# Optimization experiments

Measured on AMD Instinct MI355X. Metric: run time of the kernel, lower is better.

The kernel has to match this reference:

```python
import jax, jax.numpy as jnp
import numpy as np

N = 100000   # nodes
E = 800000   # edges
D = 64       # feature dim (input=hidden=output)
EPS = 1e-5   # BatchNorm eps


def setup_inputs() -> dict:
    key = jax.random.key(0)
    ks = jax.random.split(key, 24)
    s = 1.0 / np.sqrt(D)
    inp = {
        "x": jax.random.normal(ks[0], (N, D), jnp.float32),
        "edge_index": jax.random.randint(ks[1], (2, E), 0, N, jnp.int64),
        # GCNConv weights (x @ W + b after normalized aggregation)
        "W1": jax.random.normal(ks[2], (D, D), jnp.float32) * s,
        "b1": jax.random.normal(ks[3], (D,), jnp.float32) * 0.01,
        "W2": jax.random.normal(ks[4], (D, D), jnp.float32) * s,
        "b2": jax.random.normal(ks[5], (D,), jnp.float32) * 0.01,
        "W3": jax.random.normal(ks[6], (D, D), jnp.float32) * s,
        "b3": jax.random.normal(ks[7], (D,), jnp.float32) * 0.01,
        # BatchNorm1d (inference: running stats)
        "bn1_g": jax.random.uniform(ks[8], (D,), jnp.float32, 0.5, 1.5),
        "bn1_b": jax.random.normal(ks[9], (D,), jnp.float32) * 0.1,
        "bn1_m": jax.random.normal(ks[10], (D,), jnp.float32) * 0.1,
        "bn1_v": jax.random.uniform(ks[11], (D,), jnp.float32, 0.5, 1.5),
        "bn2_g": jax.random.uniform(ks[12], (D,), jnp.float32, 0.5, 1.5),
        "bn2_b": jax.random.normal(ks[13], (D,), jnp.float32) * 0.1,
        "bn2_m": jax.random.normal(ks[14], (D,), jnp.float32) * 0.1,
        "bn2_v": jax.random.uniform(ks[15], (D,), jnp.float32, 0.5, 1.5),
        # predictor MLP: Linear -> tanh -> (dropout=id) -> Linear
        "pW1": jax.random.normal(ks[16], (D, D), jnp.float32) * s,
        "pb1": jax.random.normal(ks[17], (D,), jnp.float32) * 0.01,
        "pW2": jax.random.normal(ks[18], (D, D), jnp.float32) * s,
        "pb2": jax.random.normal(ks[19], (D,), jnp.float32) * 0.01,
    }
    return inp


def _gcn_norm(edge_index):
    # add self loops, compute sym-normalized edge coefficients (PyG GCNConv)
    loop = jnp.arange(N, dtype=edge_index.dtype)
    src = jnp.concatenate([edge_index[0], loop])
    dst = jnp.concatenate([edge_index[1], loop])
    deg = jax.ops.segment_sum(jnp.ones(src.shape[0], jnp.float32), dst, num_segments=N)
    dis = jax.lax.rsqrt(deg)  # deg >= 1 due to self loops
    norm = dis[src] * dis[dst]
    return src, dst, norm


def _gcn_layer(x, src, dst, norm, W, b):
    h = x @ W                              # [N, D] small GEMM
    msg = h[src] * norm[:, None]           # [E+N, D] gather (memory bound)
    return jax.ops.segment_sum(msg, dst, num_segments=N) + b  # scatter-add


def _bn(x, g, b, m, v):
    return (x - m) * (g * jax.lax.rsqrt(v + EPS)) + b


def reference(x, edge_index, W1, b1, W2, b2, W3, b3,
              bn1_g, bn1_b, bn1_m, bn1_v, bn2_g, bn2_b, bn2_m, bn2_v,
              pW1, pb1, pW2, pb2):
    src, dst, norm = _gcn_norm(edge_index)
    h = _gcn_layer(x, src, dst, norm, W1, b1)
    h = jax.nn.relu(_bn(h, bn1_g, bn1_b, bn1_m, bn1_v))   # dropout = id (eval)
    h = _gcn_layer(h, src, dst, norm, W2, b2)
    h = jax.nn.relu(_bn(h, bn2_g, bn2_b, bn2_m, bn2_v))
    h = _gcn_layer(h, src, dst, norm, W3, b3)
    out = jnp.tanh(h @ pW1 + pb1) @ pW2 + pb2              # predictor MLP
    return out
```

## Files before the change

kernel.cpp:

```cpp
#include <hip/hip_runtime.h>
#include <hip/hip_fp16.h>

#define N_NODES 100000
#define N_EDGES 800000
#define DIM 64
#define BN_EPS 1e-5f
#define LDX 68
#define EDGE_CAP 1600000

__global__ __launch_bounds__(256) void k_cvt_count(const float* __restrict__ x,
                                                   __half* __restrict__ xh,
                                                   const int* __restrict__ dst,
                                                   int* __restrict__ deg) {
    int idx = blockIdx.x * blockDim.x + threadIdx.x;
    if (idx < 1600000) {
        float4 v = ((const float4*)x)[idx];
        unsigned int u0 = __half_as_ushort(__float2half(v.x));
        unsigned int u1 = __half_as_ushort(__float2half(v.y));
        unsigned int u2 = __half_as_ushort(__float2half(v.z));
        unsigned int u3 = __half_as_ushort(__float2half(v.w));
        ((uint2*)xh)[idx] = make_uint2(u0 | (u1 << 16), u2 | (u3 << 16));
    }
    if (idx < N_EDGES) atomicAdd(&deg[dst[idx]], 1);
}

__global__ __launch_bounds__(256) void k_scan_fuse(const int* __restrict__ deg,
                                                   int* __restrict__ row_off,
                                                   int* __restrict__ cursor,
                                                   float* __restrict__ dinv,
                                                   int* __restrict__ gcount,
                                                   const float* __restrict__ W3,
                                                   const float* __restrict__ b3,
                                                   const float* __restrict__ pW1,
                                                   const float* __restrict__ pb1,
                                                   float* __restrict__ W3p,
                                                   float* __restrict__ b3p) {
    int tid = threadIdx.x;
    if (blockIdx.x == 98) {
        int c = tid & 63;
        int kbase = (tid >> 6) * 16;
        for (int k = kbase; k < kbase + 16; ++k) {
            float acc = 0.f;
#pragma unroll 8
            for (int j = 0; j < 64; ++j)
                acc = fmaf(W3[k * 64 + j], pW1[j * 64 + c], acc);
            W3p[k * 64 + c] = acc;
        }
        if (tid < 64) {
            float acc = pb1[c];
#pragma unroll 8
            for (int j = 0; j < 64; ++j)
                acc = fmaf(b3[j], pW1[j * 64 + c], acc);
            b3p[c] = acc;
        }
        return;
    }
    __shared__ int sdata[256];
    __shared__ int sbase;
    int base = blockIdx.x * 1024 + tid * 4;
    int4 d = make_int4(0, 0, 0, 0);
    int4 v = make_int4(0, 0, 0, 0);
    if (base < N_NODES) {
        d = *(const int4*)(deg + base);
        v.x = (d.x + 7) & ~7;
        v.y = (d.y + 7) & ~7;
        v.z = (d.z + 7) & ~7;
        v.w = (d.w + 7) & ~7;
    }
    int tsum = v.x + v.y + v.z + v.w;
    sdata[tid] = tsum;
    __syncthreads();
    for (int off = 1; off < 256; off <<= 1) {
        int t = (tid >= off) ? sdata[tid - off] : 0;
        __syncthreads();
        sdata[tid] += t;
        __syncthreads();
    }
    if (tid == 255) sbase = atomicAdd(gcount, sdata[255]);
    __syncthreads();
    if (base >= N_NODES) return;
    int excl = sdata[tid] - tsum + sbase;
    int4 o;
    o.x = excl;
    o.y = o.x + v.x;
    o.z = o.y + v.y;
    o.w = o.z + v.z;
    *(int4*)(row_off + base) = o;
    *(int4*)(cursor + base) = o;
    float4 di;
    di.x = rsqrtf((float)(d.x + 1));
    di.y = rsqrtf((float)(d.y + 1));
    di.z = rsqrtf((float)(d.z + 1));
    di.w = rsqrtf((float)(d.w + 1));
    *(float4*)(dinv + base) = di;
}

__global__ __launch_bounds__(256) void k_build(const int* __restrict__ ei,
                                               const float* __restrict__ dinv,
                                               int* __restrict__ cursor,
                                               int2* __restrict__ edges) {
    int e = blockIdx.x * blockDim.x + threadIdx.x;
    if (e >= N_EDGES) return;
    int s = ei[e];
    int d = ei[N_EDGES + e];
    int pos = atomicAdd(&cursor[d], 1);
    edges[pos] = make_int2(s, __float_as_int(dinv[s] * dinv[d]));
}

__global__ __launch_bounds__(256) void k_aggregate(const __half* __restrict__ xin,
                                                   const int* __restrict__ row_off,
                                                   const int* __restrict__ deg,
                                                   const int2* __restrict__ edges,
                                                   const float* __restrict__ dinv,
                                                   __half* __restrict__ out) {
    int lane = threadIdx.x & 63;
    int node = blockIdx.x * 4 + (threadIdx.x >> 6);
    float di = dinv[node];
    float acc = __half2float(xin[(size_t)node * DIM + lane]) * (di * di);
    int beg = __builtin_amdgcn_readfirstlane(row_off[node]);
    int lenp = (__builtin_amdgcn_readfirstlane(deg[node]) + 7) & ~7;
    int end = beg + lenp;
    for (int k = beg; k < end; k += 8) {
        int2 e0 = edges[k + 0];
        int2 e1 = edges[k + 1];
        int2 e2 = edges[k + 2];
        int2 e3 = edges[k + 3];
        int2 e4 = edges[k + 4];
        int2 e5 = edges[k + 5];
        int2 e6 = edges[k + 6];
        int2 e7 = edges[k + 7];
        float v0 = __half2float(xin[(size_t)e0.x * DIM + lane]);
        float v1 = __half2float(xin[(size_t)e1.x * DIM + lane]);
        float v2 = __half2float(xin[(size_t)e2.x * DIM + lane]);
        float v3 = __half2float(xin[(size_t)e3.x * DIM + lane]);
        float v4 = __half2float(xin[(size_t)e4.x * DIM + lane]);
        float v5 = __half2float(xin[(size_t)e5.x * DIM + lane]);
        float v6 = __half2float(xin[(size_t)e6.x * DIM + lane]);
        float v7 = __half2float(xin[(size_t)e7.x * DIM + lane]);
        acc = fmaf(__int_as_float(e0.y), v0, acc);
        acc = fmaf(__int_as_float(e1.y), v1, acc);
        acc = fmaf(__int_as_float(e2.y), v2, acc);
        acc = fmaf(__int_as_float(e3.y), v3, acc);
        acc = fmaf(__int_as_float(e4.y), v4, acc);
        acc = fmaf(__int_as_float(e5.y), v5, acc);
        acc = fmaf(__int_as_float(e6.y), v6, acc);
        acc = fmaf(__int_as_float(e7.y), v7, acc);
    }
    out[(size_t)node * DIM + lane] = __float2half(acc);
}

#define GEMM_STEP(SX, SW)                                                      \
    {                                                                          \
        float4 a0 = *(const float4*)&SX[(r0 + 0) * LDX + k4 * 4];              \
        float4 a1 = *(const float4*)&SX[(r0 + 1) * LDX + k4 * 4];              \
        float4 a2 = *(const float4*)&SX[(r0 + 2) * LDX + k4 * 4];              \
        float4 a3 = *(const float4*)&SX[(r0 + 3) * LDX + k4 * 4];              \
        float4 b0 = *(const float4*)&SW[(k4 * 4 + 0) * 64 + c0];               \
        float4 b1 = *(const float4*)&SW[(k4 * 4 + 1) * 64 + c0];               \
        float4 b2 = *(const float4*)&SW[(k4 * 4 + 2) * 64 + c0];               \
        float4 b3 = *(const float4*)&SW[(k4 * 4 + 3) * 64 + c0];               \
        const float* ap[4] = {&a0.x, &a1.x, &a2.x, &a3.x};                     \
        _Pragma("unroll") for (int i = 0; i < 4; ++i) {                        \
            float x0 = ap[i][0], x1 = ap[i][1], x2 = ap[i][2], x3 = ap[i][3];  \
            acc[i][0] = fmaf(x0, b0.x, acc[i][0]);                             \
            acc[i][1] = fmaf(x0, b0.y, acc[i][1]);                             \
            acc[i][2] = fmaf(x0, b0.z, acc[i][2]);                             \
            acc[i][3] = fmaf(x0, b0.w, acc[i][3]);                             \
            acc[i][0] = fmaf(x1, b1.x, acc[i][0]);                             \
            acc[i][1] = fmaf(x1, b1.y, acc[i][1]);                             \
            acc[i][2] = fmaf(x1, b1.z, acc[i][2]);                             \
            acc[i][3] = fmaf(x1, b1.w, acc[i][3]);                             \
            acc[i][0] = fmaf(x2, b2.x, acc[i][0]);                             \
            acc[i][1] = fmaf(x2, b2.y, acc[i][1]);                             \
            acc[i][2] = fmaf(x2, b2.z, acc[i][2]);                             \
            acc[i][3] = fmaf(x2, b2.w, acc[i][3]);                             \
            acc[i][0] = fmaf(x3, b3.x, acc[i][0]);                             \
            acc[i][1] = fmaf(x3, b3.y, acc[i][1]);                             \
            acc[i][2] = fmaf(x3, b3.z, acc[i][2]);                             \
            acc[i][3] = fmaf(x3, b3.w, acc[i][3]);                             \
        }                                                                      \
    }

#define STAGE_H2F(SRCPTR, SXPTR)                                               \
    {                                                                          \
        int r = tid >> 2;                                                      \
        int q = tid & 3;                                                       \
        int row = row0 + r;                                                    \
        float4* dst = (float4*)(SXPTR + r * LDX);                              \
        if (row < N_NODES) {                                                   \
            const uint2* src = (const uint2*)(SRCPTR + (size_t)row * DIM);     \
            _Pragma("unroll") for (int m = 0; m < 4; ++m) {                    \
                uint2 u = src[q + m * 4];                                      \
                float4 f;                                                      \
                f.x = __half2float(__ushort_as_half((unsigned short)(u.x & 0xffff)));       \
                f.y = __half2float(__ushort_as_half((unsigned short)(u.x >> 16)));          \
                f.z = __half2float(__ushort_as_half((unsigned short)(u.y & 0xffff)));       \
                f.w = __half2float(__ushort_as_half((unsigned short)(u.y >> 16)));          \
                dst[q + m * 4] = f;                                            \
            }                                                                  \
        } else {                                                               \
            float4 z = make_float4(0.f, 0.f, 0.f, 0.f);                        \
            _Pragma("unroll") for (int m = 0; m < 4; ++m) dst[q + m * 4] = z;  \
        }                                                                      \
    }

__global__ __launch_bounds__(256) void k_gemm_bn_h(const __half* __restrict__ xin,
                                                   const float* __restrict__ W,
                                                   const float* __restrict__ bias,
                                                   const float* __restrict__ bng,
                                                   const float* __restrict__ bnb,
                                                   const float* __restrict__ bnm,
                                                   const float* __restrict__ bnv,
                                                   __half* __restrict__ out) {
    __shared__ float sW[4096];
    __shared__ float sX[64 * LDX];
    int tid = threadIdx.x;
    int row0 = blockIdx.x * 64;

    for (int i = tid; i < 1024; i += 256)
        ((float4*)sW)[i] = ((const float4*)W)[i];
    STAGE_H2F(xin, sX)
    __syncthreads();

    int cq = tid & 15, rq = tid >> 4;
    int c0 = cq * 4, r0 = rq * 4;
    float acc[4][4];
#pragma unroll
    for (int i = 0; i < 4; ++i)
#pragma unroll
        for (int j = 0; j < 4; ++j) acc[i][j] = 0.f;

#pragma unroll 4
    for (int k4 = 0; k4 < 16; ++k4) GEMM_STEP(sX, sW)

    float4 bv = *(const float4*)&bias[c0];
    float4 g = *(const float4*)&bng[c0];
    float4 bb = *(const float4*)&bnb[c0];
    float4 m = *(const float4*)&bnm[c0];
    float4 vv = *(const float4*)&bnv[c0];
    float A0 = g.x * rsqrtf(vv.x + BN_EPS);
    float A1 = g.y * rsqrtf(vv.y + BN_EPS);
    float A2 = g.z * rsqrtf(vv.z + BN_EPS);
    float A3 = g.w * rsqrtf(vv.w + BN_EPS);
    float B0 = (bv.x - m.x) * A0 + bb.x;
    float B1 = (bv.y - m.y) * A1 + bb.y;
    float B2 = (bv.z - m.z) * A2 + bb.z;
    float B3 = (bv.w - m.w) * A3 + bb.w;
#pragma unroll
    for (int i = 0; i < 4; ++i) {
        int row = row0 + r0 + i;
        if (row >= N_NODES) break;
        unsigned int u0 = __half_as_ushort(__float2half(fmaxf(0.f, fmaf(acc[i][0], A0, B0))));
        unsigned int u1 = __half_as_ushort(__float2half(fmaxf(0.f, fmaf(acc[i][1], A1, B1))));
        unsigned int u2 = __half_as_ushort(__float2half(fmaxf(0.f, fmaf(acc[i][2], A2, B2))));
        unsigned int u3 = __half_as_ushort(__float2half(fmaxf(0.f, fmaf(acc[i][3], A3, B3))));
        *(uint2*)(out + (size_t)row * DIM + c0) = make_uint2(u0 | (u1 << 16), u2 | (u3 << 16));
    }
}

__global__ __launch_bounds__(256) void k_tail(const __half* __restrict__ xin,
                                              const float* __restrict__ W3p,
                                              const float* __restrict__ b3p,
                                              const float* __restrict__ pW2,
                                              const float* __restrict__ pb2,
                                              float* __restrict__ out) {
    __shared__ float sW1[4096];
    __shared__ float sW2[4096];
    __shared__ float sX[64 * LDX];
    int tid = threadIdx.x;
    int row0 = blockIdx.x * 64;

    for (int i = tid; i < 1024; i += 256) {
        ((float4*)sW1)[i] = ((const float4*)W3p)[i];
        ((float4*)sW2)[i] = ((const float4*)pW2)[i];
    }
    STAGE_H2F(xin, sX)
    __syncthreads();

    int cq = tid & 15, rq = tid >> 4;
    int c0 = cq * 4, r0 = rq * 4;
    float acc[4][4];

#pragma unroll
    for (int i = 0; i < 4; ++i)
#pragma unroll
        for (int j = 0; j < 4; ++j) acc[i][j] = 0.f;
#pragma unroll 4
    for (int k4 = 0; k4 < 16; ++k4) GEMM_STEP(sX, sW1)
    __syncthreads();

    {
        float4 bv = *(const float4*)&b3p[c0];
#pragma unroll
        for (int i = 0; i < 4; ++i) {
            float4 h;
            h.x = tanhf(acc[i][0] + bv.x);
            h.y = tanhf(acc[i][1] + bv.y);
            h.z = tanhf(acc[i][2] + bv.z);
            h.w = tanhf(acc[i][3] + bv.w);
            *(float4*)&sX[(r0 + i) * LDX + c0] = h;
        }
    }
    __syncthreads();

#pragma unroll
    for (int i = 0; i < 4; ++i)
#pragma unroll
        for (int j = 0; j < 4; ++j) acc[i][j] = 0.f;
#pragma unroll 4
    for (int k4 = 0; k4 < 16; ++k4) GEMM_STEP(sX, sW2)

    float4 bv = *(const float4*)&pb2[c0];
#pragma unroll
    for (int i = 0; i < 4; ++i) {
        int row = row0 + r0 + i;
        if (row >= N_NODES) break;
        float4 o;
        o.x = acc[i][0] + bv.x;
        o.y = acc[i][1] + bv.y;
        o.z = acc[i][2] + bv.z;
        o.w = acc[i][3] + bv.w;
        *(float4*)(out + (size_t)row * DIM + c0) = o;
    }
}

extern "C" void kernel_launch(void* const* d_in, const int* in_sizes, int n_in,
                              void* d_out, int out_size, void* d_ws, size_t ws_size,
                              hipStream_t stream) {
    const float* x     = (const float*)d_in[0];
    const int*   ei    = (const int*)d_in[1];
    const float* W1    = (const float*)d_in[2];
    const float* b1    = (const float*)d_in[3];
    const float* W2    = (const float*)d_in[4];
    const float* b2    = (const float*)d_in[5];
    const float* W3    = (const float*)d_in[6];
    const float* b3    = (const float*)d_in[7];
    const float* bn1_g = (const float*)d_in[8];
    const float* bn1_b = (const float*)d_in[9];
    const float* bn1_m = (const float*)d_in[10];
    const float* bn1_v = (const float*)d_in[11];
    const float* bn2_g = (const float*)d_in[12];
    const float* bn2_b = (const float*)d_in[13];
    const float* bn2_m = (const float*)d_in[14];
    const float* bn2_v = (const float*)d_in[15];
    const float* pW1   = (const float*)d_in[16];
    const float* pb1   = (const float*)d_in[17];
    const float* pW2   = (const float*)d_in[18];
    const float* pb2   = (const float*)d_in[19];
    float* out = (float*)d_out;

    char* ws = (char*)d_ws;
    int*   deg      = (int*)ws;                      ws += 100352 * 4;
    int*   gcount   = (int*)ws;                      ws += 4 * 4;
    int*   row_off  = (int*)ws;                      ws += 100352 * 4;
    int*   cursor   = (int*)ws;                      ws += 100352 * 4;
    int2*  edges    = (int2*)ws;                     ws += (size_t)EDGE_CAP * 8;
    float* dinv     = (float*)ws;                    ws += 100352 * 4;
    float* W3p      = (float*)ws;                    ws += 4096 * 4;
    float* b3p      = (float*)ws;                    ws += 64 * 4;
    __half* xh      = (__half*)ws;                   ws += (size_t)N_NODES * DIM * 2;
    __half* hbuf    = (__half*)ws;                   ws += (size_t)N_NODES * DIM * 2;
    __half* abuf    = (__half*)ws;                   ws += (size_t)N_NODES * DIM * 2;

    const int blk = 256;
    int gE    = (N_EDGES + blk - 1) / blk;
    int gCvt  = 6250;
    int gAgg  = N_NODES / 4;
    int gTile = (N_NODES + 63) / 64;

    size_t zbytes = (size_t)(100352 * 3 + 4) * 4 + (size_t)EDGE_CAP * 8;
    hipMemsetAsync(deg, 0, zbytes, stream);
    k_cvt_count<<<gCvt, blk, 0, stream>>>(x, xh, ei + N_EDGES, deg);
    k_scan_fuse<<<99, blk, 0, stream>>>(deg, row_off, cursor, dinv, gcount,
                                        W3, b3, pW1, pb1, W3p, b3p);
    k_build<<<gE, blk, 0, stream>>>(ei, dinv, cursor, edges);

    k_aggregate<<<gAgg, blk, 0, stream>>>(xh, row_off, deg, edges, dinv, abuf);
    k_gemm_bn_h<<<gTile, blk, 0, stream>>>(abuf, W1, b1, bn1_g, bn1_b, bn1_m, bn1_v, hbuf);

    k_aggregate<<<gAgg, blk, 0, stream>>>(hbuf, row_off, deg, edges, dinv, abuf);
    k_gemm_bn_h<<<gTile, blk, 0, stream>>>(abuf, W2, b2, bn2_g, bn2_b, bn2_m, bn2_v, hbuf);

    k_aggregate<<<gAgg, blk, 0, stream>>>(hbuf, row_off, deg, edges, dinv, abuf);
    k_tail<<<gTile, blk, 0, stream>>>(abuf, W3p, b3p, pW2, pb2, out);
}
```

Measured before the change: 372.9 us.

## Factor symmetric GCN normalization into node scaling and shrink edge list to indices

Splits the symmetric edge weight dinv[s]*dinv[d] into per-node factors. Source features are pre-scaled by dinv, in the build kernel for the input and in the GEMM epilogue for hidden layers, and each aggregate result is multiplied by dinv[dst] once. The edge list then stores only a source index (offset by one so padded zero entries point at a zeroed sentinel row), halving edge bytes read in each of three aggregations and turning per-edge FMAs into adds. It adds an extra scaling pass over the input features, pads the feature buffers by a row, and uses separate ping-pong hidden buffers.

```diff
diff --git a/kernel.cpp b/kernel.cpp
--- a/kernel.cpp
+++ b/kernel.cpp
@@ -7,6 +7,7 @@
 #define BN_EPS 1e-5f
 #define LDX 68
 #define EDGE_CAP 1600000
+
 
 __global__ __launch_bounds__(256) void k_cvt_count(const float* __restrict__ x,
                                                    __half* __restrict__ xh,
@@ -19,8 +20,10 @@
         unsigned int u1 = __half_as_ushort(__float2half(v.y));
         unsigned int u2 = __half_as_ushort(__float2half(v.z));
         unsigned int u3 = __half_as_ushort(__float2half(v.w));
-        ((uint2*)xh)[idx] = make_uint2(u0 | (u1 << 16), u2 | (u3 << 16));
-    }
+        ((uint2*)(xh + DIM))[idx] = make_uint2(u0 | (u1 << 16), u2 | (u3 << 16));
+    }
+    if (blockIdx.x == 0 && threadIdx.x < 16)
+        ((uint2*)xh)[threadIdx.x] = make_uint2(0u, 0u);
     if (idx < N_EDGES) atomicAdd(&deg[dst[idx]], 1);
 }
 
@@ -95,58 +98,69 @@
     *(float4*)(dinv + base) = di;
 }
 
-__global__ __launch_bounds__(256) void k_build(const int* __restrict__ ei,
-                                               const float* __restrict__ dinv,
-                                               int* __restrict__ cursor,
-                                               int2* __restrict__ edges) {
-    int e = blockIdx.x * blockDim.x + threadIdx.x;
-    if (e >= N_EDGES) return;
-    int s = ei[e];
-    int d = ei[N_EDGES + e];
-    int pos = atomicAdd(&cursor[d], 1);
-    edges[pos] = make_int2(s, __float_as_int(dinv[s] * dinv[d]));
+__global__ __launch_bounds__(256) void k_build_scale(const int* __restrict__ ei,
+                                                     int* __restrict__ cursor,
+                                                     int* __restrict__ edges,
+                                                     const float* __restrict__ dinv,
+                                                     __half* __restrict__ xh) {
+    int b = blockIdx.x;
+    int tid = threadIdx.x;
+    if (b < 3125) {
+        int e = b * 256 + tid;
+        if (e >= N_EDGES) return;
+        int s = ei[e];
+        int d = ei[N_EDGES + e];
+        int pos = atomicAdd(&cursor[d], 1);
+        edges[pos] = s + 1;
+    } else {
+        int idx = (b - 3125) * 256 + tid;
+        int row = idx >> 4;
+        float dv = dinv[row];
+        uint2 u = ((uint2*)(xh + DIM))[idx];
+        float f0 = __half2float(__ushort_as_half((unsigned short)(u.x & 0xffff))) * dv;
+        float f1 = __half2float(__ushort_as_half((unsigned short)(u.x >> 16))) * dv;
+        float f2 = __half2float(__ushort_as_half((unsigned short)(u.y & 0xffff))) * dv;
+        float f3 = __half2float(__ushort_as_half((unsigned short)(u.y >> 16))) * dv;
+        unsigned int u0 = __half_as_ushort(__float2half(f0));
+        unsigned int u1 = __half_as_ushort(__float2half(f1));
+        unsigned int u2 = __half_as_ushort(__float2half(f2));
+        unsigned int u3 = __half_as_ushort(__float2half(f3));
+        ((uint2*)(xh + DIM))[idx] = make_uint2(u0 | (u1 << 16), u2 | (u3 << 16));
+    }
 }
 
 __global__ __launch_bounds__(256) void k_aggregate(const __half* __restrict__ xin,
                                                    const int* __restrict__ row_off,
                                                    const int* __restrict__ deg,
-                                                   const int2* __restrict__ edges,
+                                                   const int* __restrict__ edges,
                                                    const float* __restrict__ dinv,
                                                    __half* __restrict__ out) {
     int lane = threadIdx.x & 63;
     int node = blockIdx.x * 4 + (threadIdx.x >> 6);
-    float di = dinv[node];
-    float acc = __half2float(xin[(size_t)node * DIM + lane]) * (di * di);
+    float acc = __half2float(xin[(size_t)(node + 1) * DIM + lane]);
     int beg = __builtin_amdgcn_readfirstlane(row_off[node]);
     int lenp = (__builtin_amdgcn_readfirstlane(deg[node]) + 7) & ~7;
     int end = beg + lenp;
     for (int k = beg; k < end; k += 8) {
-        int2 e0 = edges[k + 0];
-        int2 e1 = edges[k + 1];
-        int2 e2 = edges[k + 2];
-        int2 e3 = edges[k + 3];
-        int2 e4 = edges[k + 4];
-        int2 e5 = edges[k + 5];
-        int2 e6 = edges[k + 6];
-        int2 e7 = edges[k + 7];
-        float v0 = __half2float(xin[(size_t)e0.x * DIM + lane]);
-        float v1 = __half2float(xin[(size_t)e1.x * DIM + lane]);
-        float v2 = __half2float(xin[(size_t)e2.x * DIM + lane]);
-        float v3 = __half2float(xin[(size_t)e3.x * DIM + lane]);
-        float v4 = __half2float(xin[(size_t)e4.x * DIM + lane]);
-        float v5 = __half2float(xin[(size_t)e5.x * DIM + lane]);
-        float v6 = __half2float(xin[(size_t)e6.x * DIM + lane]);
-        float v7 = __half2float(xin[(size_t)e7.x * DIM + lane]);
-        acc = fmaf(__int_as_float(e0.y), v0, acc);
-        acc = fmaf(__int_as_float(e1.y), v1, acc);
-        acc = fmaf(__int_as_float(e2.y), v2, acc);
-        acc = fmaf(__int_as_float(e3.y), v3, acc);
-        acc = fmaf(__int_as_float(e4.y), v4, acc);
-        acc = fmaf(__int_as_float(e5.y), v5, acc);
-        acc = fmaf(__int_as_float(e6.y), v6, acc);
-        acc = fmaf(__int_as_float(e7.y), v7, acc);
-    }
-    out[(size_t)node * DIM + lane] = __float2half(acc);
+        int e0 = edges[k + 0];
+        int e1 = edges[k + 1];
+        int e2 = edges[k + 2];
+        int e3 = edges[k + 3];
+        int e4 = edges[k + 4];
+        int e5 = edges[k + 5];
+        int e6 = edges[k + 6];
+        int e7 = edges[k + 7];
+        float v0 = __half2float(xin[(size_t)e0 * DIM + lane]);
+        float v1 = __half2float(xin[(size_t)e1 * DIM + lane]);
+        float v2 = __half2float(xin[(size_t)e2 * DIM + lane]);
+        float v3 = __half2float(xin[(size_t)e3 * DIM + lane]);
+        float v4 = __half2float(xin[(size_t)e4 * DIM + lane]);
+        float v5 = __half2float(xin[(size_t)e5 * DIM + lane]);
+        float v6 = __half2float(xin[(size_t)e6 * DIM + lane]);
+        float v7 = __half2float(xin[(size_t)e7 * DIM + lane]);
+        acc += ((v0 + v1) + (v2 + v3)) + ((v4 + v5) + (v6 + v7));
+    }
+    out[(size_t)node * DIM + lane] = __float2half(dinv[node] * acc);
 }
 
 #define GEMM_STEP(SX, SW)                                                      \
@@ -211,11 +225,15 @@
                                                    const float* __restrict__ bnb,
                                                    const float* __restrict__ bnm,
                                                    const float* __restrict__ bnv,
+                                                   const float* __restrict__ dinv,
                                                    __half* __restrict__ out) {
     __shared__ float sW[4096];
     __shared__ float sX[64 * LDX];
     int tid = threadIdx.x;
     int row0 = blockIdx.x * 64;
+
+    if (blockIdx.x == 0 && tid < 16)
+        ((uint2*)out)[tid] = make_uint2(0u, 0u);
 
     for (int i = tid; i < 1024; i += 256)
         ((float4*)sW)[i] = ((const float4*)W)[i];
@@ -250,11 +268,12 @@
     for (int i = 0; i < 4; ++i) {
         int row = row0 + r0 + i;
         if (row >= N_NODES) break;
-        unsigned int u0 = __half_as_ushort(__float2half(fmaxf(0.f, fmaf(acc[i][0], A0, B0))));
-        unsigned int u1 = __half_as_ushort(__float2half(fmaxf(0.f, fmaf(acc[i][1], A1, B1))));
-        unsigned int u2 = __half_as_ushort(__float2half(fmaxf(0.f, fmaf(acc[i][2], A2, B2))));
-        unsigned int u3 = __half_as_ushort(__float2half(fmaxf(0.f, fmaf(acc[i][3], A3, B3))));
-        *(uint2*)(out + (size_t)row * DIM + c0) = make_uint2(u0 | (u1 << 16), u2 | (u3 << 16));
+        float dv = dinv[row];
+        unsigned int u0 = __half_as_ushort(__float2half(fmaxf(0.f, fmaf(acc[i][0], A0, B0)) * dv));
+        unsigned int u1 = __half_as_ushort(__float2half(fmaxf(0.f, fmaf(acc[i][1], A1, B1)) * dv));
+        unsigned int u2 = __half_as_ushort(__float2half(fmaxf(0.f, fmaf(acc[i][2], A2, B2)) * dv));
+        unsigned int u3 = __half_as_ushort(__float2half(fmaxf(0.f, fmaf(acc[i][3], A3, B3)) * dv));
+        *(uint2*)(out + (size_t)(row + 1) * DIM + c0) = make_uint2(u0 | (u1 << 16), u2 | (u3 << 16));
     }
 }
 
@@ -350,37 +369,38 @@
     float* out = (float*)d_out;
 
     char* ws = (char*)d_ws;
-    int*   deg      = (int*)ws;                      ws += 100352 * 4;
-    int*   gcount   = (int*)ws;                      ws += 4 * 4;
-    int*   row_off  = (int*)ws;                      ws += 100352 * 4;
-    int*   cursor   = (int*)ws;                      ws += 100352 * 4;
-    int2*  edges    = (int2*)ws;                     ws += (size_t)EDGE_CAP * 8;
-    float* dinv     = (float*)ws;                    ws += 100352 * 4;
-    float* W3p      = (float*)ws;                    ws += 4096 * 4;
-    float* b3p      = (float*)ws;                    ws += 64 * 4;
-    __half* xh      = (__half*)ws;                   ws += (size_t)N_NODES * DIM * 2;
-    __half* hbuf    = (__half*)ws;                   ws += (size_t)N_NODES * DIM * 2;
+    int*    deg     = (int*)ws;                      ws += 100352 * 4;
+    int*    gcount  = (int*)ws;                      ws += 4 * 4;
+    int*    row_off = (int*)ws;                      ws += 100352 * 4;
+    int*    cursor  = (int*)ws;                      ws += 100352 * 4;
+    int*    edges   = (int*)ws;                      ws += (size_t)EDGE_CAP * 4;
+    float*  dinv    = (float*)ws;                    ws += 100352 * 4;
+    float*  W3p     = (float*)ws;                    ws += 4096 * 4;
+    float*  b3p     = (float*)ws;                    ws += 64 * 4;
+    __half* xh      = (__half*)ws;                   ws += (size_t)(N_NODES + 4) * DIM * 2;
+    __half* hbufA   = (__half*)ws;                   ws += (size_t)(N_NODES + 4) * DIM * 2;
+    __half* hbufB   = (__half*)ws;                   ws += (size_t)(N_NODES + 4) * DIM * 2;
     __half* abuf    = (__half*)ws;                   ws += (size_t)N_NODES * DIM * 2;
 
     const int blk = 256;
-    int gE    = (N_EDGES + blk - 1) / blk;
     int gCvt  = 6250;
+    int gBS   = 3125 + 6250;
     int gAgg  = N_NODES / 4;
     int gTile = (N_NODES + 63) / 64;
 
-    size_t zbytes = (size_t)(100352 * 3 + 4) * 4 + (size_t)EDGE_CAP * 8;
+    size_t zbytes = (size_t)(100352 * 3 + 4) * 4 + (size_t)EDGE_CAP * 4;
     hipMemsetAsync(deg, 0, zbytes, stream);
     k_cvt_count<<<gCvt, blk, 0, stream>>>(x, xh, ei + N_EDGES, deg);
     k_scan_fuse<<<99, blk, 0, stream>>>(deg, row_off, cursor, dinv, gcount,
                                         W3, b3, pW1, pb1, W3p, b3p);
-    k_build<<<gE, blk, 0, stream>>>(ei, dinv, cursor, edges);
+    k_build_scale<<<gBS, blk, 0, stream>>>(ei, cursor, edges, dinv, xh);
 
     k_aggregate<<<gAgg, blk, 0, stream>>>(xh, row_off, deg, edges, dinv, abuf);
-    k_gemm_bn_h<<<gTile, blk, 0, stream>>>(abuf, W1, b1, bn1_g, bn1_b, bn1_m, bn1_v, hbuf);
-
-    k_aggregate<<<gAgg, blk, 0, stream>>>(hbuf, row_off, deg, edges, dinv, abuf);
-    k_gemm_bn_h<<<gTile, blk, 0, stream>>>(abuf, W2, b2, bn2_g, bn2_b, bn2_m, bn2_v, hbuf);
-
-    k_aggregate<<<gAgg, blk, 0, stream>>>(hbuf, row_off, deg, edges, dinv, abuf);
+    k_gemm_bn_h<<<gTile, blk, 0, stream>>>(abuf, W1, b1, bn1_g, bn1_b, bn1_m, bn1_v, dinv, hbufA);
+
+    k_aggregate<<<gAgg, blk, 0, stream>>>(hbufA, row_off, deg, edges, dinv, abuf);
+    k_gemm_bn_h<<<gTile, blk, 0, stream>>>(abuf, W2, b2, bn2_g, bn2_b, bn2_m, bn2_v, dinv, hbufB);
+
+    k_aggregate<<<gAgg, blk, 0, stream>>>(hbufB, row_off, deg, edges, dinv, abuf);
     k_tail<<<gTile, blk, 0, stream>>>(abuf, W3p, b3p, pW2, pb2, out);
 }
```

New measurement: 384.8 us. 1.03x slower.
